# Kernel optimization log

Hardware: AMD Instinct MI355X
Metric: run time of the kernel (lower is better)

The kernel has to match this reference:

```python
import jax, jax.numpy as jnp
import numpy as np

B = 128
N_IN = 32      # n_inp_capsules
D_IN = 8       # dim_inp_capsules
N_OUT = 10     # n_out_capsules
D_OUT = 16     # dim_out_capsules
DIM = 12       # dim_input (spatial side)
N = N_IN * DIM * DIM  # 4608 total input capsule positions
NUM_ROUTING = 3


def setup_inputs() -> dict:
    key = jax.random.key(0)
    k1, k2 = jax.random.split(key)
    x = jax.random.normal(k1, (B, D_IN, N_IN, DIM, DIM), dtype=jnp.float32)
    weight = jax.random.normal(k2, (D_IN, D_OUT, N, N_OUT), dtype=jnp.float32)
    return {"x": x, "weight": weight}


def squash(s, axis):
    # s_sq/(1+s_sq) * s / sqrt(s_sq)  -- exactly the module's squash (no eps)
    s_sq = jnp.sum(s * s, axis=axis, keepdims=True)
    return s_sq / (1.0 + s_sq) * s / jnp.sqrt(s_sq)


def reference(x, weight):
    b_sz = x.shape[0]
    # view(B, C, -1).permute(0,2,1): (B, N, D_IN)
    u = x.reshape(b_sz, D_IN, -1).transpose(0, 2, 1)
    # u_hat[b,o,n,j] = sum_d u[b,n,d] * weight[d,o,n,j]  (replaces the double python loop)
    u_hat = jnp.einsum('bnd,donj->bonj', u, weight)  # (B, D_OUT, N, N_OUT)
    b = jnp.zeros((b_sz, 1, N, N_OUT), dtype=u_hat.dtype)
    s = None
    for _ in range(NUM_ROUTING):
        c = jax.nn.softmax(b, axis=3)                      # over output capsules
        s = squash(jnp.sum(u_hat * c, axis=2), axis=1)     # (B, D_OUT, N_OUT)
        b = b + jnp.sum(s[:, :, None, :] * u_hat, axis=1, keepdims=True)
    return s  # torch returns s.squeeze() of (B, D_OUT, 1, N_OUT) -> (B, D_OUT, N_OUT)
```

## Files before the change

### kernel.cpp

```cpp
#include <hip/hip_runtime.h>
#include <math.h>

#define NTOT 4608

typedef _Float16 f16;
typedef _Float16 f16x4 __attribute__((ext_vector_type(4)));
typedef _Float16 f16x8 __attribute__((ext_vector_type(8)));
typedef float f32x4 __attribute__((ext_vector_type(4)));

__global__ __launch_bounds__(320) void prep(const float* __restrict__ x, const float* __restrict__ W,
                                            f16* __restrict__ ut, f16* __restrict__ wt) {
    __shared__ float l[2560];
    const int k = threadIdx.x;
    if (blockIdx.x < 2304) {
        const int n0 = blockIdx.x * 2;
        #pragma unroll
        for (int r = 0; r < 8; ++r) {
            const int f = k + r * 320;
            const int p = f / 20, q = f - p * 20;
            l[f] = W[(size_t)p * 46080 + n0 * 10 + q];
        }
        __syncthreads();
        const int half = k / 160, rr = k - half * 160;
        const int j = rr >> 4, o = rr & 15;
        f16x8 v;
        #pragma unroll
        for (int d = 0; d < 8; ++d)
            v[d] = (f16)l[d * 320 + o * 20 + half * 10 + j];
        *reinterpret_cast<f16x8*>(wt + ((size_t)(n0 + half) * 160 + rr) * 8) = v;
    } else {
        const int t = (blockIdx.x - 2304) * 320 + k;
        if (t < 128 * NTOT) {
            const int b = t / NTOT, n = t - b * NTOT;
            f16x8 v;
            #pragma unroll
            for (int d = 0; d < 8; ++d)
                v[d] = (f16)x[((size_t)b * 8 + d) * NTOT + n];
            *reinterpret_cast<f16x8*>(ut + (size_t)t * 8) = v;
        }
    }
}

__global__ __launch_bounds__(256) void kernelA(const f16* __restrict__ ut, const f16* __restrict__ wt,
                                               f16* __restrict__ uh, float* __restrict__ partial) {
    __shared__ float s0t[4][16][164];
    const int tid = threadIdx.x, w = tid >> 6, lane = tid & 63;
    const int col = lane & 15, qA = lane >> 4;
    const int chunk = blockIdx.x, bg = blockIdx.y, b0 = bg * 16;
    const int b = b0 + col;
    const int nstart = chunk * 32 + w * 8;

    const f16* ab = wt + ((size_t)nstart * 160 + col) * 8;
    const f16* ub = ut + ((size_t)b * NTOT + nstart) * 8;
    f16* uhw = uh + (size_t)nstart * 20480 + (size_t)(qA >> 1) * 1024 + b * 8 + (qA & 1) * 4;

    const f32x4 cz = {0.f, 0.f, 0.f, 0.f};
    f32x4 s0a[10];
    #pragma unroll
    for (int m = 0; m < 10; ++m) s0a[m] = cz;

    for (int nl = 0; nl < 8; ++nl) {
        const f16x8 bf = *reinterpret_cast<const f16x8*>(ub + nl * 8);
        #pragma unroll
        for (int m = 0; m < 10; ++m) {
            const f16x8 af = *reinterpret_cast<const f16x8*>(ab + ((size_t)nl * 160 + m * 16) * 8);
            f32x4 C = __builtin_amdgcn_mfma_f32_16x16x32_f16(af, bf, cz, 0, 0, 0);
            s0a[m] += C;
            f16x4 hv;
            hv[0] = (f16)(0.25f * C[0]); hv[1] = (f16)(0.25f * C[1]);
            hv[2] = (f16)(0.25f * C[2]); hv[3] = (f16)(0.25f * C[3]);
            *reinterpret_cast<f16x4*>(uhw + (size_t)nl * 20480 + m * 2048) = hv;
        }
    }

    #pragma unroll
    for (int m = 0; m < 10; ++m)
        *reinterpret_cast<f32x4*>(&s0t[w][col][m * 16 + qA * 4]) = s0a[m];
    __syncthreads();
    for (int r = tid; r < 2560; r += 256) {
        const int row = r / 160, slot = r - row * 160;
        float v = s0t[0][row][slot] + s0t[1][row][slot] + s0t[2][row][slot] + s0t[3][row][slot];
        partial[((size_t)chunk * 128 + b0 + row) * 160 + slot] = v;
    }
}

__global__ __launch_bounds__(256) void kernelB(const f16* __restrict__ uh, const float* __restrict__ Ar,
                                               float* __restrict__ partial) {
    __shared__ float s1t[4][16][164];
    const int tid = threadIdx.x, w = tid >> 6, lane = tid & 63;
    const int g = lane & 15, q = lane >> 4;
    const int chunk = blockIdx.x, bg = blockIdx.y;
    const int b = bg * 16 + g;
    const int nstart = chunk * 32 + w * 8;
    const bool qlow = (q < 2);

    float Af[5][8];
    #pragma unroll
    for (int s = 0; s < 5; ++s) {
        f32x4 a0 = *reinterpret_cast<const f32x4*>(Ar + (size_t)b * 160 + (4 * s + q) * 8);
        f32x4 a1 = *reinterpret_cast<const f32x4*>(Ar + (size_t)b * 160 + (4 * s + q) * 8 + 4);
        #pragma unroll
        for (int t = 0; t < 4; ++t) { Af[s][t] = a0[t]; Af[s][4 + t] = a1[t]; }
    }

    float P[5][8];
    #pragma unroll
    for (int s = 0; s < 5; ++s)
        #pragma unroll
        for (int t = 0; t < 8; ++t) P[s][t] = 0.f;

    const f16* uhb = uh + (size_t)nstart * 20480 + (size_t)q * 1024 + b * 8;

    for (int nl = 0; nl < 8; ++nl) {
        f16x8 U[5];
        #pragma unroll
        for (int s = 0; s < 5; ++s)
            U[s] = *reinterpret_cast<const f16x8*>(uhb + (size_t)nl * 20480 + s * 4096);

        float tp[5];
        #pragma unroll
        for (int s = 0; s < 5; ++s) {
            float acc = 0.f;
            #pragma unroll
            for (int t = 0; t < 8; ++t)
                acc = fmaf(Af[s][t], (float)U[s][t], acc);
            tp[s] = acc;
        }

        float tt[10];
        #pragma unroll
        for (int s = 0; s < 5; ++s) {
            float tq = tp[s] + __shfl_xor(tp[s], 16, 64);
            float tr = __shfl_xor(tq, 32, 64);
            tt[2 * s]     = qlow ? tq : tr;
            tt[2 * s + 1] = qlow ? tr : tq;
        }

        float mx = fmaxf(fmaxf(fmaxf(fmaxf(tt[0], tt[1]), fmaxf(tt[2], tt[3])),
                               fmaxf(fmaxf(tt[4], tt[5]), fmaxf(tt[6], tt[7]))),
                         fmaxf(tt[8], tt[9]));
        float c[10], sum = 0.f;
        #pragma unroll
        for (int j = 0; j < 10; ++j) { float e = __expf(tt[j] - mx); c[j] = e; sum += e; }
        const float inv = 1.0f / sum;

        #pragma unroll
        for (int s = 0; s < 5; ++s) {
            const float cm = (qlow ? c[2 * s] : c[2 * s + 1]) * inv;
            #pragma unroll
            for (int t = 0; t < 8; ++t)
                P[s][t] = fmaf(cm, (float)U[s][t], P[s][t]);
        }
    }

    #pragma unroll
    for (int s = 0; s < 5; ++s) {
        const int sg = 4 * s + q;
        f32x4 p0 = {P[s][0], P[s][1], P[s][2], P[s][3]};
        f32x4 p1 = {P[s][4], P[s][5], P[s][6], P[s][7]};
        *reinterpret_cast<f32x4*>(&s1t[w][g][sg * 8])     = p0;
        *reinterpret_cast<f32x4*>(&s1t[w][g][sg * 8 + 4]) = p1;
    }
    __syncthreads();
    for (int r = tid; r < 2560; r += 256) {
        const int row = r / 160, slot = r - row * 160;
        float v = s1t[0][row][slot] + s1t[1][row][slot] + s1t[2][row][slot] + s1t[3][row][slot];
        partial[((size_t)chunk * 128 + bg * 16 + row) * 160 + slot] = v;
    }
}

template<int MODE>
__global__ __launch_bounds__(640) void reduce_squash(const float* __restrict__ partial,
                                                     float* __restrict__ Ar, float* __restrict__ out,
                                                     float sumscale) {
    const int b = blockIdx.x;
    const int k = threadIdx.x % 160;
    const int r = threadIdx.x / 160;
    __shared__ float red[4][160];
    float acc = 0.f;
    for (int c = r; c < 144; c += 4)
        acc += partial[((size_t)c * 128 + b) * 160 + k];
    red[r][k] = acc;
    __syncthreads();
    if (r == 0) {
        float a = (red[0][k] + red[1][k] + red[2][k] + red[3][k]) * sumscale;
        red[0][k] = a;
        __syncthreads();
        const int j = k >> 4;
        float ssq = 0.f;
        #pragma unroll
        for (int o = 0; o < 16; ++o) { float v = red[0][j * 16 + o]; ssq = fmaf(v, v, ssq); }
        const float s = a * ssq / ((1.f + ssq) * sqrtf(ssq));
        if (MODE == 0)      Ar[(size_t)b * 160 + k] = s;
        else if (MODE == 1) Ar[(size_t)b * 160 + k] += s;
        else { const int o = k & 15; out[(size_t)b * 160 + o * 10 + j] = s; }
    } else {
        __syncthreads();
    }
}

extern "C" void kernel_launch(void* const* d_in, const int* in_sizes, int n_in,
                              void* d_out, int out_size, void* d_ws, size_t ws_size,
                              hipStream_t stream) {
    const float* x = (const float*)d_in[0];
    const float* W = (const float*)d_in[1];
    float* out = (float*)d_out;

    f16* ut = (f16*)d_ws;
    f16* wt = ut + (size_t)128 * NTOT * 8;
    f16* uh = wt + (size_t)NTOT * 160 * 8;
    float* Ar = (float*)(uh + (size_t)NTOT * 20 * 128 * 8);
    float* partial = Ar + 128 * 160;

    prep<<<2304 + 1844, 320, 0, stream>>>(x, W, ut, wt);

    dim3 gA(144, 8);
    kernelA<<<gA, 256, 0, stream>>>(ut, wt, uh, partial);
    reduce_squash<0><<<128, 640, 0, stream>>>(partial, Ar, out, 0.025f);

    kernelB<<<gA, 256, 0, stream>>>(uh, Ar, partial);
    reduce_squash<1><<<128, 640, 0, stream>>>(partial, Ar, out, 1.0f);

    kernelB<<<gA, 256, 0, stream>>>(uh, Ar, partial);
    reduce_squash<2><<<128, 640, 0, stream>>>(partial, Ar, out, 1.0f);
}
```

Measured before the change: 166.0 us.

## Use nontemporal u_hat traffic, alternate kernelB chunk order, split reduce_squash blocks

Stores u_hat in kernelA and loads it in kernelB with nontemporal hints. The first kernelB pass walks chunks in descending order so it starts on the chunks the previous kernel touched last, which may still be in the last-level cache, and the second pass walks them ascending. reduce_squash is split into two blocks per batch (five output capsules each) to double the grid and halve the block size. Nontemporal hints may keep data out of cache that the next pass could reuse, so the net effect on u_hat reuse across passes is uncertain.

```diff
diff --git a/kernel.cpp b/kernel.cpp
--- a/kernel.cpp
+++ b/kernel.cpp
@@ -7,6 +7,18 @@
 typedef _Float16 f16x4 __attribute__((ext_vector_type(4)));
 typedef _Float16 f16x8 __attribute__((ext_vector_type(8)));
 typedef float f32x4 __attribute__((ext_vector_type(4)));
+typedef unsigned int u32x2 __attribute__((ext_vector_type(2)));
+typedef unsigned int u32x4 __attribute__((ext_vector_type(4)));
+
+__device__ __forceinline__ void nt_store8(void* p, f16x4 v) {
+    u32x2 u; __builtin_memcpy(&u, &v, 8);
+    __builtin_nontemporal_store(u, (u32x2*)p);
+}
+__device__ __forceinline__ f16x8 nt_load16(const void* p) {
+    u32x4 u = __builtin_nontemporal_load((const u32x4*)p);
+    f16x8 v; __builtin_memcpy(&v, &u, 16);
+    return v;
+}
 
 __global__ __launch_bounds__(320) void prep(const float* __restrict__ x, const float* __restrict__ W,
                                             f16* __restrict__ ut, f16* __restrict__ wt) {
@@ -69,7 +81,7 @@
             f16x4 hv;
             hv[0] = (f16)(0.25f * C[0]); hv[1] = (f16)(0.25f * C[1]);
             hv[2] = (f16)(0.25f * C[2]); hv[3] = (f16)(0.25f * C[3]);
-            *reinterpret_cast<f16x4*>(uhw + (size_t)nl * 20480 + m * 2048) = hv;
+            nt_store8(uhw + (size_t)nl * 20480 + m * 2048, hv);
         }
     }
 
@@ -84,12 +96,12 @@
     }
 }
 
-__global__ __launch_bounds__(256) void kernelB(const f16* __restrict__ uh, const float* __restrict__ Ar,
-                                               float* __restrict__ partial) {
+__device__ __forceinline__ void kernelB_impl(const f16* __restrict__ uh, const float* __restrict__ Ar,
+                                             float* __restrict__ partial, int chunk) {
     __shared__ float s1t[4][16][164];
     const int tid = threadIdx.x, w = tid >> 6, lane = tid & 63;
     const int g = lane & 15, q = lane >> 4;
-    const int chunk = blockIdx.x, bg = blockIdx.y;
+    const int bg = blockIdx.y;
     const int b = bg * 16 + g;
     const int nstart = chunk * 32 + w * 8;
     const bool qlow = (q < 2);
@@ -115,7 +127,7 @@
         f16x8 U[5];
         #pragma unroll
         for (int s = 0; s < 5; ++s)
-            U[s] = *reinterpret_cast<const f16x8*>(uhb + (size_t)nl * 20480 + s * 4096);
+            U[s] = nt_load16(uhb + (size_t)nl * 20480 + s * 4096);
 
         float tp[5];
         #pragma unroll
@@ -169,33 +181,40 @@
     }
 }
 
+template<bool DESC>
+__global__ __launch_bounds__(256) void kernelB(const f16* __restrict__ uh, const float* __restrict__ Ar,
+                                               float* __restrict__ partial) {
+    const int chunk = DESC ? (143 - (int)blockIdx.x) : (int)blockIdx.x;
+    kernelB_impl(uh, Ar, partial, chunk);
+}
+
 template<int MODE>
-__global__ __launch_bounds__(640) void reduce_squash(const float* __restrict__ partial,
+__global__ __launch_bounds__(320) void reduce_squash(const float* __restrict__ partial,
                                                      float* __restrict__ Ar, float* __restrict__ out,
                                                      float sumscale) {
-    const int b = blockIdx.x;
-    const int k = threadIdx.x % 160;
-    const int r = threadIdx.x / 160;
-    __shared__ float red[4][160];
+    const int b = blockIdx.x, jh = blockIdx.y;
+    const int k2 = threadIdx.x % 80;
+    const int r  = threadIdx.x / 80;
+    const int jp = k2 >> 4, o = k2 & 15;
+    const int j  = jh * 5 + jp;
+    const int slot = j * 16 + o;
+    __shared__ float red[4][80];
+    __shared__ float srs[80];
     float acc = 0.f;
     for (int c = r; c < 144; c += 4)
-        acc += partial[((size_t)c * 128 + b) * 160 + k];
-    red[r][k] = acc;
+        acc += partial[((size_t)c * 128 + b) * 160 + slot];
+    red[r][k2] = acc;
+    __syncthreads();
+    if (r == 0) srs[k2] = (red[0][k2] + red[1][k2] + red[2][k2] + red[3][k2]) * sumscale;
     __syncthreads();
     if (r == 0) {
-        float a = (red[0][k] + red[1][k] + red[2][k] + red[3][k]) * sumscale;
-        red[0][k] = a;
-        __syncthreads();
-        const int j = k >> 4;
         float ssq = 0.f;
         #pragma unroll
-        for (int o = 0; o < 16; ++o) { float v = red[0][j * 16 + o]; ssq = fmaf(v, v, ssq); }
-        const float s = a * ssq / ((1.f + ssq) * sqrtf(ssq));
-        if (MODE == 0)      Ar[(size_t)b * 160 + k] = s;
-        else if (MODE == 1) Ar[(size_t)b * 160 + k] += s;
-        else { const int o = k & 15; out[(size_t)b * 160 + o * 10 + j] = s; }
-    } else {
-        __syncthreads();
+        for (int oo = 0; oo < 16; ++oo) { float v = srs[jp * 16 + oo]; ssq = fmaf(v, v, ssq); }
+        const float s = srs[k2] * ssq / ((1.f + ssq) * sqrtf(ssq));
+        if (MODE == 0)      Ar[(size_t)b * 160 + slot] = s;
+        else if (MODE == 1) Ar[(size_t)b * 160 + slot] += s;
+        else                out[(size_t)b * 160 + o * 10 + j] = s;
     }
 }
 
@@ -214,13 +233,13 @@
 
     prep<<<2304 + 1844, 320, 0, stream>>>(x, W, ut, wt);
 
-    dim3 gA(144, 8);
+    dim3 gA(144, 8), gRS(128, 2);
     kernelA<<<gA, 256, 0, stream>>>(ut, wt, uh, partial);
-    reduce_squash<0><<<128, 640, 0, stream>>>(partial, Ar, out, 0.025f);
-
-    kernelB<<<gA, 256, 0, stream>>>(uh, Ar, partial);
-    reduce_squash<1><<<128, 640, 0, stream>>>(partial, Ar, out, 1.0f);
-
-    kernelB<<<gA, 256, 0, stream>>>(uh, Ar, partial);
-    reduce_squash<2><<<128, 640, 0, stream>>>(partial, Ar, out, 1.0f);
-}
+    reduce_squash<0><<<gRS, 320, 0, stream>>>(partial, Ar, out, 0.025f);
+
+    kernelB<true ><<<gA, 256, 0, stream>>>(uh, Ar, partial);
+    reduce_squash<1><<<gRS, 320, 0, stream>>>(partial, Ar, out, 1.0f);
+
+    kernelB<false><<<gA, 256, 0, stream>>>(uh, Ar, partial);
+    reduce_squash<2><<<gRS, 320, 0, stream>>>(partial, Ar, out, 1.0f);
+}
```

New measurement: 179.8 us. 1.08x slower.
